# Kernel optimization log

Hardware: AMD Instinct MI355X
Metric: run time of the kernel (lower is better)

Reference implementation:

```python
import jax, jax.numpy as jnp
import numpy as np

SCALE = 0.125  # 1/sqrt(d_head)
QLEN, KLEN, BSZ, NHEAD, DHEAD = 1024, 1024, 4, 16, 64
RLEN = KLEN + 1


def rel_shift(x, klen):
    # x: [q, r, b, n] -> relative shift -> [q, klen, b, n]
    q, r, b, n = x.shape
    x = x.reshape(r, q, b, n)[1:]
    x = x.reshape(q, r - 1, b, n)[:, :klen]
    return x


def setup_inputs() -> dict:
    key = jax.random.key(0)
    ks = jax.random.split(key, 9)
    q_head = jax.random.normal(ks[0], (QLEN, BSZ, NHEAD, DHEAD), jnp.float32)
    k_head_h = jax.random.normal(ks[1], (KLEN, BSZ, NHEAD, DHEAD), jnp.float32)
    v_head_h = jax.random.normal(ks[2], (KLEN, BSZ, NHEAD, DHEAD), jnp.float32)
    k_head_r = jax.random.normal(ks[3], (RLEN, BSZ, NHEAD, DHEAD), jnp.float32)
    seg_embed = jax.random.normal(ks[4], (2, NHEAD, DHEAD), jnp.float32)
    seg_mat = jax.random.randint(ks[5], (QLEN, KLEN, BSZ), 0, 2) > 0  # bool
    r_w_bias = jax.random.normal(ks[6], (NHEAD, DHEAD), jnp.float32) * 0.02
    r_r_bias = jax.random.normal(ks[7], (NHEAD, DHEAD), jnp.float32) * 0.02
    r_s_bias = jax.random.normal(ks[8], (NHEAD, DHEAD), jnp.float32) * 0.02
    # causal mask: 1.0 where key position j is after query position i
    i = jnp.arange(QLEN)[:, None]
    j = jnp.arange(KLEN)[None, :]
    attn_mask = (j > i).astype(jnp.float32).reshape(QLEN, KLEN, 1, 1)
    return {
        "q_head": q_head, "k_head_h": k_head_h, "v_head_h": v_head_h,
        "k_head_r": k_head_r, "seg_embed": seg_embed, "seg_mat": seg_mat,
        "r_w_bias": r_w_bias, "r_r_bias": r_r_bias, "r_s_bias": r_s_bias,
        "attn_mask": attn_mask,
    }


def reference(q_head, k_head_h, v_head_h, k_head_r, seg_embed, seg_mat,
              r_w_bias, r_r_bias, r_s_bias, attn_mask):
    # content-based score: [q, k, b, n]
    ac = jnp.einsum('ibnd,jbnd->ijbn', q_head + r_w_bias, k_head_h)
    # position-based score, then relative shift
    bd = jnp.einsum('ibnd,jbnd->ijbn', q_head + r_r_bias, k_head_r)
    bd = rel_shift(bd, klen=ac.shape[1])
    # segment-based score: [q, 2, b, n] -> select same/diff per (i,j,b)
    ef = jnp.einsum('ibnd,snd->isbn', q_head + r_s_bias, seg_embed)
    ef = jnp.where(seg_mat[..., None], ef[:, 1:2], ef[:, 0:1])  # [q,k,b,n]
    attn_score = (ac + bd + ef) * SCALE
    attn_score = attn_score - 1e30 * attn_mask
    attn_prob = jax.nn.softmax(attn_score, axis=1)  # softmax over key axis j
    attn_vec = jnp.einsum('ijbn,jbnd->ibnd', attn_prob, v_head_h)
    return attn_vec
```

## Files before the change

### kernel.cpp

```cpp
#include <hip/hip_runtime.h>

#define QLEN  1024
#define KLEN  1024
#define BSZ   4
#define NHEAD 16
#define DHEAD 64
#define PS    4096
#define SCALE 0.125f
#define MSHIFT 16.0f

#define WK 72
#define WR 72
#define WV 68
#define WP 68

typedef __attribute__((ext_vector_type(8))) short  short8;
typedef __attribute__((ext_vector_type(4))) short  short4v;
typedef __attribute__((ext_vector_type(4))) float  float4v;

union S8 { short8 v; short4v h[2]; unsigned short u[8]; };

__device__ __forceinline__ unsigned short f2b(float f) {
    unsigned u; __builtin_memcpy(&u, &f, 4);
    return (unsigned short)((u + 0x8000u) >> 16);
}
__device__ __forceinline__ float b2f(unsigned short s) {
    unsigned u = ((unsigned)s) << 16;
    float f; __builtin_memcpy(&f, &u, 4);
    return f;
}

#define MFMA(a,b,c) __builtin_amdgcn_mfma_f32_16x16x32_bf16((a),(b),(c),0,0,0)

__global__ __launch_bounds__(256)
void seg_pack(const int4* __restrict__ sm4, unsigned long long* __restrict__ bits)
{
    int w  = (blockIdx.x << 2) + (threadIdx.x >> 6);
    int i  = w >> 4;
    int jw = w & 15;
    int jj = threadIdx.x & 63;
    int4 v = sm4[i*KLEN + (jw << 6) + jj];
    unsigned long long m0 = __ballot(v.x != 0);
    unsigned long long m1 = __ballot(v.y != 0);
    unsigned long long m2 = __ballot(v.z != 0);
    unsigned long long m3 = __ballot(v.w != 0);
    if (jj == 0) {
        unsigned long long* p = bits + (i << 6) + jw;
        p[0] = m0; p[16] = m1; p[32] = m2; p[48] = m3;
    }
}

__global__ __launch_bounds__(256, 3)
void relattn_mfma10(const float* __restrict__ q,
                    const float* __restrict__ kh,
                    const float* __restrict__ vh,
                    const float* __restrict__ kr,
                    const float* __restrict__ seg_embed,
                    const unsigned long long* __restrict__ segbits,
                    const float* __restrict__ rw,
                    const float* __restrict__ rr,
                    const float* __restrict__ rs,
                    float* __restrict__ out)
{
    __shared__ __align__(16) unsigned short sK [64*WK];
    __shared__ __align__(16) unsigned short sKr[128*WR];
    __shared__ __align__(16) unsigned short sVt[64*WV];
    __shared__ __align__(16) unsigned short sBD[64*WP];

    const int tid  = threadIdx.x;
    const int lane = tid & 63;
    const int wave = tid >> 6;
    const int quad = lane >> 4;
    const int l16  = lane & 15;
    const int bx   = blockIdx.x;
    const int h    = blockIdx.y;
    const int b    = h >> 4;
    const int n    = h & 15;
    const int qt   = (b & 1) ? bx : (15 - bx);
    const int i0   = qt << 6;
    const int m0   = wave << 4;
    const int hoff = h << 6;
    const int d0   = quad << 3;
    const int G0   = 961 - i0;
    const int srow = tid >> 4;
    const int c4   = (tid & 15) << 2;

    S8 aw0, aw1, ar0, ar1;
    float ef0r[4], ef1r[4];
    {
        float qv[16], rwv[16], rrv[16], rsv[16];
        const float* qp = q + (i0 + m0 + l16)*PS + hoff;
        *(float4*)&qv[0]  = *(const float4*)(qp + d0);
        *(float4*)&qv[4]  = *(const float4*)(qp + d0 + 4);
        *(float4*)&qv[8]  = *(const float4*)(qp + 32 + d0);
        *(float4*)&qv[12] = *(const float4*)(qp + 32 + d0 + 4);
        const float* rwp = rw + n*DHEAD;
        *(float4*)&rwv[0]  = *(const float4*)(rwp + d0);
        *(float4*)&rwv[4]  = *(const float4*)(rwp + d0 + 4);
        *(float4*)&rwv[8]  = *(const float4*)(rwp + 32 + d0);
        *(float4*)&rwv[12] = *(const float4*)(rwp + 32 + d0 + 4);
        const float* rrp = rr + n*DHEAD;
        *(float4*)&rrv[0]  = *(const float4*)(rrp + d0);
        *(float4*)&rrv[4]  = *(const float4*)(rrp + d0 + 4);
        *(float4*)&rrv[8]  = *(const float4*)(rrp + 32 + d0);
        *(float4*)&rrv[12] = *(const float4*)(rrp + 32 + d0 + 4);
        const float* rsp = rs + n*DHEAD;
        *(float4*)&rsv[0]  = *(const float4*)(rsp + d0);
        *(float4*)&rsv[4]  = *(const float4*)(rsp + d0 + 4);
        *(float4*)&rsv[8]  = *(const float4*)(rsp + 32 + d0);
        *(float4*)&rsv[12] = *(const float4*)(rsp + 32 + d0 + 4);

        #pragma unroll
        for (int mm = 0; mm < 8; ++mm) {
            aw0.u[mm] = f2b(qv[mm]   + rwv[mm]);
            aw1.u[mm] = f2b(qv[8+mm] + rwv[8+mm]);
            ar0.u[mm] = f2b(qv[mm]   + rrv[mm]);
            ar1.u[mm] = f2b(qv[8+mm] + rrv[8+mm]);
        }
        const float* se0 = seg_embed + n*DHEAD;
        const float* se1 = seg_embed + (NHEAD + n)*DHEAD;
        float e0 = 0.f, e1 = 0.f;
        #pragma unroll
        for (int mm = 0; mm < 8; ++mm) {
            float qs = qv[mm] + rsv[mm];
            e0 += qs * se0[d0 + mm];  e1 += qs * se1[d0 + mm];
            float qs2 = qv[8+mm] + rsv[8+mm];
            e0 += qs2 * se0[32 + d0 + mm];  e1 += qs2 * se1[32 + d0 + mm];
        }
        e0 += __shfl_xor(e0, 16); e0 += __shfl_xor(e0, 32);
        e1 += __shfl_xor(e1, 16); e1 += __shfl_xor(e1, 32);
        #pragma unroll
        for (int r = 0; r < 4; ++r) {
            ef0r[r] = __shfl(e0, (quad << 2) + r);
            ef1r[r] = __shfl(e1, (quad << 2) + r);
        }
    }

    {
        float4 t0[4], t1[4];
        #pragma unroll
        for (int k2 = 0; k2 < 4; ++k2) {
            int row = srow + (k2 << 4);
            t0[k2] = *(const float4*)(kh + row*PS + hoff + c4);
            t1[k2] = *(const float4*)(vh + row*PS + hoff + c4);
        }
        #pragma unroll
        for (int k2 = 0; k2 < 4; ++k2) {
            int row = srow + (k2 << 4);
            float4 kv = t0[k2];
            short4v kb = {(short)f2b(kv.x),(short)f2b(kv.y),(short)f2b(kv.z),(short)f2b(kv.w)};
            *(short4v*)&sK[row*WK + c4] = kb;
            float4 vv = t1[k2];
            sVt[(c4+0)*WV + row] = f2b(vv.x);
            sVt[(c4+1)*WV + row] = f2b(vv.y);
            sVt[(c4+2)*WV + row] = f2b(vv.z);
            sVt[(c4+3)*WV + row] = f2b(vv.w);
        }
    }
    {
        const float4 zf4 = make_float4(0.f, 0.f, 0.f, 0.f);
        float4 t0[4], t1[4];
        #pragma unroll
        for (int k2 = 0; k2 < 4; ++k2) {
            int row = srow + (k2 << 4);
            int g1 = G0 + row;
            t0[k2] = (g1 <= 1024) ? *(const float4*)(kr + g1*PS + hoff + c4) : zf4;
            int g2 = G0 + 64 + row;
            t1[k2] = (g2 <= 1024) ? *(const float4*)(kr + g2*PS + hoff + c4) : zf4;
        }
        #pragma unroll
        for (int k2 = 0; k2 < 4; ++k2) {
            int row = srow + (k2 << 4);
            float4 r1 = t0[k2];
            short4v rb1 = {(short)f2b(r1.x),(short)f2b(r1.y),(short)f2b(r1.z),(short)f2b(r1.w)};
            *(short4v*)&sKr[row*WR + c4] = rb1;
            float4 r2 = t1[k2];
            short4v rb2 = {(short)f2b(r2.x),(short)f2b(r2.y),(short)f2b(r2.z),(short)f2b(r2.w)};
            *(short4v*)&sKr[(64 + row)*WR + c4] = rb2;
        }
    }
    __syncthreads();

    float lp[4];
    float4v Ov[4];
    #pragma unroll
    for (int r = 0; r < 4; ++r) lp[r] = 0.f;
    #pragma unroll
    for (int cb = 0; cb < 4; ++cb) Ov[cb] = (float4v){0.f,0.f,0.f,0.f};

    for (int jt = 0; jt <= qt; ++jt) {
        const int  j0   = jt << 6;
        const bool diag = (jt == qt);
        const bool more = (jt < qt);
        const int  rot  = (jt & 1) << 2;

        float4 pK[4], pV[4], pR[4];
        if (more) {
            const int j0n = j0 + 64;
            const float4 zf4l = make_float4(0.f, 0.f, 0.f, 0.f);
            #pragma unroll
            for (int k2 = 0; k2 < 4; ++k2) {
                int row = srow + (k2 << 4);
                pK[k2] = *(const float4*)(kh + (j0n + row)*PS + hoff + c4);
                pV[k2] = *(const float4*)(vh + (j0n + row)*PS + hoff + c4);
                int g = G0 + ((jt + 2) << 6) + row;
                pR[k2] = (g <= 1024) ? *(const float4*)(kr + g*PS + hoff + c4) : zf4l;
            }
        }
        unsigned long long wbits[4];
        #pragma unroll
        for (int r = 0; r < 4; ++r) {
            int il = m0 + (quad << 2) + r;
            wbits[r] = segbits[(((i0+il) << 2) + b)*16 + jt] >> l16;
        }

        const int bbHi = diag ? wave : 3;
        float4v ac[4];
        #pragma unroll
        for (int bb = 0; bb < 4; ++bb) {
            ac[bb] = (float4v){0.f,0.f,0.f,0.f};
            if (bb <= bbHi) {
                const unsigned short* kp = &sK[((bb<<4) + l16)*WK + d0];
                short8 b0 = *(const short8*)kp;
                short8 b1 = *(const short8*)(kp + 32);
                ac[bb] = MFMA(aw0.v, b0, ac[bb]);
                ac[bb] = MFMA(aw1.v, b1, ac[bb]);
            }
        }

        const int cbLo = 3 - wave;
        const int cbHi = diag ? 3 : (7 - wave);
        #pragma unroll
        for (int cb = 0; cb < 8; ++cb) {
            if (cb >= cbLo && cb <= cbHi) {
                const unsigned short* rp = &sKr[((((cb + rot) & 7) << 4) + l16)*WR + d0];
                short8 b0 = *(const short8*)rp;
                short8 b1 = *(const short8*)(rp + 32);
                float4v z = (float4v){0.f,0.f,0.f,0.f};
                z = MFMA(ar0.v, b0, z);
                z = MFMA(ar1.v, b1, z);
                #pragma unroll
                for (int r = 0; r < 4; ++r) {
                    int il = m0 + (quad << 2) + r;
                    int jl = (cb << 4) + l16 - 63 + il;
                    if (jl >= 0 && jl < 64)
                        sBD[il*WP + jl] = f2b(z[r]);
                }
            }
        }

        #pragma unroll
        for (int r = 0; r < 4; ++r) {
            const int il = m0 + (quad << 2) + r;
            float psum = 0.f;
            #pragma unroll
            for (int bb = 0; bb < 4; ++bb) {
                const int jl = (bb << 4) + l16;
                float bd = b2f(sBD[il*WP + jl]);
                float ef = ((wbits[r] >> (bb << 4)) & 1ull) ? ef1r[r] : ef0r[r];
                float s  = (ac[bb][r] + bd + ef) * SCALE - MSHIFT;
                if (j0 + jl > i0 + il) s = -1e30f;
                float p = __expf(s);
                psum += p;
                sBD[il*WP + jl] = f2b(p);
            }
            lp[r] += psum;
        }

        {
            const unsigned short* pr = &sBD[(m0 + l16)*WP + d0];
            S8 pa0, pa1;
            pa0.h[0] = *(const short4v*)pr;
            pa0.h[1] = *(const short4v*)(pr + 4);
            pa1.h[0] = *(const short4v*)(pr + 32);
            pa1.h[1] = *(const short4v*)(pr + 36);
            const bool k2on = !(diag && wave < 2);
            #pragma unroll
            for (int cb = 0; cb < 4; ++cb) {
                const unsigned short* vp = &sVt[((cb<<4) + l16)*WV + d0];
                S8 v0, v1;
                v0.h[0] = *(const short4v*)vp;
                v0.h[1] = *(const short4v*)(vp + 4);
                Ov[cb] = MFMA(pa0.v, v0.v, Ov[cb]);
                if (k2on) {
                    v1.h[0] = *(const short4v*)(vp + 32);
                    v1.h[1] = *(const short4v*)(vp + 36);
                    Ov[cb] = MFMA(pa1.v, v1.v, Ov[cb]);
                }
            }
        }

        if (more) {
            __syncthreads();
            const int krslot = (jt & 1) << 6;
            #pragma unroll
            for (int k2 = 0; k2 < 4; ++k2) {
                int row = srow + (k2 << 4);
                float4 kv = pK[k2];
                short4v kb = {(short)f2b(kv.x),(short)f2b(kv.y),(short)f2b(kv.z),(short)f2b(kv.w)};
                *(short4v*)&sK[row*WK + c4] = kb;
                float4 vv = pV[k2];
                sVt[(c4+0)*WV + row] = f2b(vv.x);
                sVt[(c4+1)*WV + row] = f2b(vv.y);
                sVt[(c4+2)*WV + row] = f2b(vv.z);
                sVt[(c4+3)*WV + row] = f2b(vv.w);
                float4 rv = pR[k2];
                short4v rb = {(short)f2b(rv.x),(short)f2b(rv.y),(short)f2b(rv.z),(short)f2b(rv.w)};
                *(short4v*)&sKr[(krslot + row)*WR + c4] = rb;
            }
            __syncthreads();
        }
    }

    #pragma unroll
    for (int r = 0; r < 4; ++r) {
        float l = lp[r];
        l += __shfl_xor(l, 1);
        l += __shfl_xor(l, 2);
        l += __shfl_xor(l, 4);
        l += __shfl_xor(l, 8);
        const float inv = 1.f / l;
        const int il = m0 + (quad << 2) + r;
        #pragma unroll
        for (int cb = 0; cb < 4; ++cb)
            out[(i0+il)*PS + hoff + (cb<<4) + l16] = Ov[cb][r] * inv;
    }
}

extern "C" void kernel_launch(void* const* d_in, const int* in_sizes, int n_in,
                              void* d_out, int out_size, void* d_ws, size_t ws_size,
                              hipStream_t stream)
{
    const float* q  = (const float*)d_in[0];
    const float* kh = (const float*)d_in[1];
    const float* vh = (const float*)d_in[2];
    const float* kr = (const float*)d_in[3];
    const float* se = (const float*)d_in[4];
    const int*   sm = (const int*)  d_in[5];
    const float* rw = (const float*)d_in[6];
    const float* rr = (const float*)d_in[7];
    const float* rs = (const float*)d_in[8];
    float* o = (float*)d_out;
    unsigned long long* bits = (unsigned long long*)d_ws;
    (void)in_sizes; (void)n_in; (void)out_size; (void)ws_size;

    seg_pack<<<dim3(QLEN*16/4), 256, 0, stream>>>((const int4*)sm, bits);

    dim3 grid(QLEN/64, BSZ*NHEAD);
    relattn_mfma10<<<grid, 256, 0, stream>>>(q, kh, vh, kr, se, bits, rw, rr, rs, o);
}
```

Before: 290.1 us.

## Split long causal query tiles across two blocks with atomic combine and separate normalization

The attention kernel now uses a 1D grid of 1792 blocks. A lookup table assigns each block a query tile and, for tiles with qt>=4, one half of the key range. Split blocks accumulate unnormalized outputs and row sums with atomicAdd into buffers that seg_pack pre-zeroes, and a new norm_div kernel divides by the sums afterwards. The aim is better load balance under the causal triangle and shorter critical-path blocks. The cost is extra atomic traffic, a third kernel pass over the output, and redundant setup work in split blocks. It relies on the fixed MSHIFT softmax offset, so no max-rescaling between halves is needed.

```diff
diff --git a/kernel.cpp b/kernel.cpp
--- a/kernel.cpp
+++ b/kernel.cpp
@@ -32,8 +32,12 @@
 
 #define MFMA(a,b,c) __builtin_amdgcn_mfma_f32_16x16x32_bf16((a),(b),(c),0,0,0)
 
+__device__ const signed char QT_TAB[28] = {15,15,14,12, 13,13,14,10, 9,11,11,12, 7,9,8,2, 6,7,8,10, 5,6,1,3, 5,0,4,4};
+__device__ const signed char CH_TAB[28] = { 0, 1, 1, 1,  0, 1, 0, 1, 0, 0, 1, 0, 0,1,1,0, 1,1,0, 0, 0,0,0,0, 1,0,0,1};
+
 __global__ __launch_bounds__(256)
-void seg_pack(const int4* __restrict__ sm4, unsigned long long* __restrict__ bits)
+void seg_pack(const int4* __restrict__ sm4, unsigned long long* __restrict__ bits,
+              float4* __restrict__ out4, float4* __restrict__ lp4)
 {
     int w  = (blockIdx.x << 2) + (threadIdx.x >> 6);
     int i  = w >> 4;
@@ -48,10 +52,26 @@
         unsigned long long* p = bits + (i << 6) + jw;
         p[0] = m0; p[16] = m1; p[32] = m2; p[48] = m3;
     }
+    const float4 z4 = make_float4(0.f, 0.f, 0.f, 0.f);
+    out4[(blockIdx.x << 8) + threadIdx.x] = z4;
+    if (blockIdx.x < 64) lp4[(blockIdx.x << 8) + threadIdx.x] = z4;
+}
+
+__global__ __launch_bounds__(256)
+void norm_div(float4* __restrict__ out4, const float* __restrict__ lp)
+{
+    int idx = (blockIdx.x << 8) + threadIdx.x;
+    int i   = idx >> 10;
+    int col = (idx & 1023) << 2;
+    float l = lp[(i << 6) + (col >> 6)];
+    float4 v = out4[idx];
+    float inv = 1.f / l;
+    v.x *= inv; v.y *= inv; v.z *= inv; v.w *= inv;
+    out4[idx] = v;
 }
 
 __global__ __launch_bounds__(256, 3)
-void relattn_mfma10(const float* __restrict__ q,
+void relattn_mfma13(const float* __restrict__ q,
                     const float* __restrict__ kh,
                     const float* __restrict__ vh,
                     const float* __restrict__ kr,
@@ -60,7 +80,8 @@
                     const float* __restrict__ rw,
                     const float* __restrict__ rr,
                     const float* __restrict__ rs,
-                    float* __restrict__ out)
+                    float* __restrict__ out,
+                    float* __restrict__ lpart)
 {
     __shared__ __align__(16) unsigned short sK [64*WK];
     __shared__ __align__(16) unsigned short sKr[128*WR];
@@ -72,11 +93,20 @@
     const int wave = tid >> 6;
     const int quad = lane >> 4;
     const int l16  = lane & 15;
-    const int bx   = blockIdx.x;
-    const int h    = blockIdx.y;
-    const int b    = h >> 4;
-    const int n    = h & 15;
-    const int qt   = (b & 1) ? bx : (15 - bx);
+
+    const int id = blockIdx.x;
+    const int h  = id & 63;
+    const int s  = id >> 6;
+    const int b  = h >> 4;
+    const int n  = h & 15;
+
+    const int  qt   = QT_TAB[s];
+    const int  ch   = CH_TAB[s];
+    const bool dual = (qt >= 4);
+    const int  sp   = (qt + 1) >> 1;
+    const int  jt0  = (dual && ch)  ? sp       : 0;
+    const int  jtN  = (dual && !ch) ? (sp - 1) : qt;
+
     const int i0   = qt << 6;
     const int m0   = wave << 4;
     const int hoff = h << 6;
@@ -137,12 +167,13 @@
     }
 
     {
+        const int j0s = jt0 << 6;
         float4 t0[4], t1[4];
         #pragma unroll
         for (int k2 = 0; k2 < 4; ++k2) {
             int row = srow + (k2 << 4);
-            t0[k2] = *(const float4*)(kh + row*PS + hoff + c4);
-            t1[k2] = *(const float4*)(vh + row*PS + hoff + c4);
+            t0[k2] = *(const float4*)(kh + (j0s + row)*PS + hoff + c4);
+            t1[k2] = *(const float4*)(vh + (j0s + row)*PS + hoff + c4);
         }
         #pragma unroll
         for (int k2 = 0; k2 < 4; ++k2) {
@@ -159,13 +190,15 @@
     }
     {
         const float4 zf4 = make_float4(0.f, 0.f, 0.f, 0.f);
+        const int slotLo = (jt0 & 1) << 6;
+        const int slotHi = 64 - slotLo;
         float4 t0[4], t1[4];
         #pragma unroll
         for (int k2 = 0; k2 < 4; ++k2) {
             int row = srow + (k2 << 4);
-            int g1 = G0 + row;
+            int g1 = G0 + (jt0 << 6) + row;
             t0[k2] = (g1 <= 1024) ? *(const float4*)(kr + g1*PS + hoff + c4) : zf4;
-            int g2 = G0 + 64 + row;
+            int g2 = g1 + 64;
             t1[k2] = (g2 <= 1024) ? *(const float4*)(kr + g2*PS + hoff + c4) : zf4;
         }
         #pragma unroll
@@ -173,25 +206,25 @@
             int row = srow + (k2 << 4);
             float4 r1 = t0[k2];
             short4v rb1 = {(short)f2b(r1.x),(short)f2b(r1.y),(short)f2b(r1.z),(short)f2b(r1.w)};
-            *(short4v*)&sKr[row*WR + c4] = rb1;
+            *(short4v*)&sKr[(slotLo + row)*WR + c4] = rb1;
             float4 r2 = t1[k2];
             short4v rb2 = {(short)f2b(r2.x),(short)f2b(r2.y),(short)f2b(r2.z),(short)f2b(r2.w)};
-            *(short4v*)&sKr[(64 + row)*WR + c4] = rb2;
+            *(short4v*)&sKr[(slotHi + row)*WR + c4] = rb2;
         }
     }
     __syncthreads();
 
-    float lp[4];
+    float lsum[4];
     float4v Ov[4];
     #pragma unroll
-    for (int r = 0; r < 4; ++r) lp[r] = 0.f;
+    for (int r = 0; r < 4; ++r) lsum[r] = 0.f;
     #pragma unroll
     for (int cb = 0; cb < 4; ++cb) Ov[cb] = (float4v){0.f,0.f,0.f,0.f};
 
-    for (int jt = 0; jt <= qt; ++jt) {
+    for (int jt = jt0; jt <= jtN; ++jt) {
         const int  j0   = jt << 6;
         const bool diag = (jt == qt);
-        const bool more = (jt < qt);
+        const bool more = (jt < jtN);
         const int  rot  = (jt & 1) << 2;
 
         float4 pK[4], pV[4], pR[4];
@@ -258,13 +291,13 @@
                 const int jl = (bb << 4) + l16;
                 float bd = b2f(sBD[il*WP + jl]);
                 float ef = ((wbits[r] >> (bb << 4)) & 1ull) ? ef1r[r] : ef0r[r];
-                float s  = (ac[bb][r] + bd + ef) * SCALE - MSHIFT;
-                if (j0 + jl > i0 + il) s = -1e30f;
-                float p = __expf(s);
+                float s2 = (ac[bb][r] + bd + ef) * SCALE - MSHIFT;
+                if (j0 + jl > i0 + il) s2 = -1e30f;
+                float p = __expf(s2);
                 psum += p;
                 sBD[il*WP + jl] = f2b(p);
             }
-            lp[r] += psum;
+            lsum[r] += psum;
         }
 
         {
@@ -314,16 +347,21 @@
 
     #pragma unroll
     for (int r = 0; r < 4; ++r) {
-        float l = lp[r];
+        float l = lsum[r];
         l += __shfl_xor(l, 1);
         l += __shfl_xor(l, 2);
         l += __shfl_xor(l, 4);
         l += __shfl_xor(l, 8);
-        const float inv = 1.f / l;
         const int il = m0 + (quad << 2) + r;
-        #pragma unroll
-        for (int cb = 0; cb < 4; ++cb)
-            out[(i0+il)*PS + hoff + (cb<<4) + l16] = Ov[cb][r] * inv;
+        if (l16 == 0) {
+            float* lpp = lpart + (((i0 + il) << 6) + h);
+            if (dual) atomicAdd(lpp, l); else *lpp = l;
+        }
+        #pragma unroll
+        for (int cb = 0; cb < 4; ++cb) {
+            float* op = out + (i0+il)*PS + hoff + (cb<<4) + l16;
+            if (dual) atomicAdd(op, Ov[cb][r]); else *op = Ov[cb][r];
+        }
     }
 }
 
@@ -342,10 +380,14 @@
     const float* rs = (const float*)d_in[8];
     float* o = (float*)d_out;
     unsigned long long* bits = (unsigned long long*)d_ws;
+    float* lpart = (float*)((char*)d_ws + 524288);
     (void)in_sizes; (void)n_in; (void)out_size; (void)ws_size;
 
-    seg_pack<<<dim3(QLEN*16/4), 256, 0, stream>>>((const int4*)sm, bits);
-
-    dim3 grid(QLEN/64, BSZ*NHEAD);
-    relattn_mfma10<<<grid, 256, 0, stream>>>(q, kh, vh, kr, se, bits, rw, rr, rs, o);
-}
+    seg_pack<<<dim3(4096), 256, 0, stream>>>((const int4*)sm, bits,
+                                             (float4*)o, (float4*)lpart);
+
+    relattn_mfma13<<<dim3(1792), 256, 0, stream>>>(q, kh, vh, kr, se, bits,
+                                                   rw, rr, rs, o, lpart);
+
+    norm_div<<<dim3(4096), 256, 0, stream>>>((float4*)o, lpart);
+}
```

Result: slower. 320.6 us (+10.5%).

## Double-buffer K/V tiles and triple-buffer Kr to drop a per-tile barrier

Applied to the files above, without the earlier changes.

Splits the K and V shared tiles into ping-pong buffers and extends the relative-key buffer to three 64-row slots with rotating indices. The next tile can then be written without first waiting for all waves to finish reading the current one, removing one __syncthreads per iteration. The cost is more LDS per block and a launch bound lowered from 3 to 2 blocks, which reduces occupancy.

```diff
diff --git a/kernel.cpp b/kernel.cpp
--- a/kernel.cpp
+++ b/kernel.cpp
@@ -50,8 +50,8 @@
     }
 }
 
-__global__ __launch_bounds__(256, 3)
-void relattn_mfma10(const float* __restrict__ q,
+__global__ __launch_bounds__(256, 2)
+void relattn_mfma14(const float* __restrict__ q,
                     const float* __restrict__ kh,
                     const float* __restrict__ vh,
                     const float* __restrict__ kr,
@@ -62,9 +62,11 @@
                     const float* __restrict__ rs,
                     float* __restrict__ out)
 {
-    __shared__ __align__(16) unsigned short sK [64*WK];
-    __shared__ __align__(16) unsigned short sKr[128*WR];
-    __shared__ __align__(16) unsigned short sVt[64*WV];
+    __shared__ __align__(16) unsigned short sK0[64*WK];
+    __shared__ __align__(16) unsigned short sK1[64*WK];
+    __shared__ __align__(16) unsigned short sKr[192*WR];
+    __shared__ __align__(16) unsigned short sV0[64*WV];
+    __shared__ __align__(16) unsigned short sV1[64*WV];
     __shared__ __align__(16) unsigned short sBD[64*WP];
 
     const int tid  = threadIdx.x;
@@ -149,12 +151,12 @@
             int row = srow + (k2 << 4);
             float4 kv = t0[k2];
             short4v kb = {(short)f2b(kv.x),(short)f2b(kv.y),(short)f2b(kv.z),(short)f2b(kv.w)};
-            *(short4v*)&sK[row*WK + c4] = kb;
+            *(short4v*)&sK0[row*WK + c4] = kb;
             float4 vv = t1[k2];
-            sVt[(c4+0)*WV + row] = f2b(vv.x);
-            sVt[(c4+1)*WV + row] = f2b(vv.y);
-            sVt[(c4+2)*WV + row] = f2b(vv.z);
-            sVt[(c4+3)*WV + row] = f2b(vv.w);
+            sV0[(c4+0)*WV + row] = f2b(vv.x);
+            sV0[(c4+1)*WV + row] = f2b(vv.y);
+            sV0[(c4+2)*WV + row] = f2b(vv.z);
+            sV0[(c4+3)*WV + row] = f2b(vv.w);
         }
     }
     {
@@ -188,11 +190,19 @@
     #pragma unroll
     for (int cb = 0; cb < 4; ++cb) Ov[cb] = (float4v){0.f,0.f,0.f,0.f};
 
+    bool cur = false;
+    int  s0  = 0;
+
     for (int jt = 0; jt <= qt; ++jt) {
         const int  j0   = jt << 6;
         const bool diag = (jt == qt);
         const bool more = (jt < qt);
-        const int  rot  = (jt & 1) << 2;
+        unsigned short* sKc = cur ? sK1 : sK0;
+        unsigned short* sVc = cur ? sV1 : sV0;
+        unsigned short* sKn = cur ? sK0 : sK1;
+        unsigned short* sVn = cur ? sV0 : sV1;
+        const int sHi = (s0 == 2) ? 0 : s0 + 1;
+        const int s2  = (s0 == 0) ? 2 : s0 - 1;
 
         float4 pK[4], pV[4], pR[4];
         if (more) {
@@ -220,7 +230,7 @@
         for (int bb = 0; bb < 4; ++bb) {
             ac[bb] = (float4v){0.f,0.f,0.f,0.f};
             if (bb <= bbHi) {
-                const unsigned short* kp = &sK[((bb<<4) + l16)*WK + d0];
+                const unsigned short* kp = &sKc[((bb<<4) + l16)*WK + d0];
                 short8 b0 = *(const short8*)kp;
                 short8 b1 = *(const short8*)(kp + 32);
                 ac[bb] = MFMA(aw0.v, b0, ac[bb]);
@@ -233,7 +243,9 @@
         #pragma unroll
         for (int cb = 0; cb < 8; ++cb) {
             if (cb >= cbLo && cb <= cbHi) {
-                const unsigned short* rp = &sKr[((((cb + rot) & 7) << 4) + l16)*WR + d0];
+                const int slot = (cb < 4) ? s0 : sHi;
+                const int rrow = (slot << 6) + ((cb & 3) << 4) + l16;
+                const unsigned short* rp = &sKr[rrow*WR + d0];
                 short8 b0 = *(const short8*)rp;
                 short8 b1 = *(const short8*)(rp + 32);
                 float4v z = (float4v){0.f,0.f,0.f,0.f};
@@ -277,7 +289,7 @@
             const bool k2on = !(diag && wave < 2);
             #pragma unroll
             for (int cb = 0; cb < 4; ++cb) {
-                const unsigned short* vp = &sVt[((cb<<4) + l16)*WV + d0];
+                const unsigned short* vp = &sVc[((cb<<4) + l16)*WV + d0];
                 S8 v0, v1;
                 v0.h[0] = *(const short4v*)vp;
                 v0.h[1] = *(const short4v*)(vp + 4);
@@ -291,25 +303,25 @@
         }
 
         if (more) {
-            __syncthreads();
-            const int krslot = (jt & 1) << 6;
             #pragma unroll
             for (int k2 = 0; k2 < 4; ++k2) {
                 int row = srow + (k2 << 4);
                 float4 kv = pK[k2];
                 short4v kb = {(short)f2b(kv.x),(short)f2b(kv.y),(short)f2b(kv.z),(short)f2b(kv.w)};
-                *(short4v*)&sK[row*WK + c4] = kb;
+                *(short4v*)&sKn[row*WK + c4] = kb;
                 float4 vv = pV[k2];
-                sVt[(c4+0)*WV + row] = f2b(vv.x);
-                sVt[(c4+1)*WV + row] = f2b(vv.y);
-                sVt[(c4+2)*WV + row] = f2b(vv.z);
-                sVt[(c4+3)*WV + row] = f2b(vv.w);
+                sVn[(c4+0)*WV + row] = f2b(vv.x);
+                sVn[(c4+1)*WV + row] = f2b(vv.y);
+                sVn[(c4+2)*WV + row] = f2b(vv.z);
+                sVn[(c4+3)*WV + row] = f2b(vv.w);
                 float4 rv = pR[k2];
                 short4v rb = {(short)f2b(rv.x),(short)f2b(rv.y),(short)f2b(rv.z),(short)f2b(rv.w)};
-                *(short4v*)&sKr[(krslot + row)*WR + c4] = rb;
+                *(short4v*)&sKr[(( s2 << 6) + row)*WR + c4] = rb;
             }
             __syncthreads();
         }
+        cur = !cur;
+        s0  = (s0 == 2) ? 0 : s0 + 1;
     }
 
     #pragma unroll
@@ -347,5 +359,5 @@
     seg_pack<<<dim3(QLEN*16/4), 256, 0, stream>>>((const int4*)sm, bits);
 
     dim3 grid(QLEN/64, BSZ*NHEAD);
-    relattn_mfma10<<<grid, 256, 0, stream>>>(q, kh, vh, kr, se, bits, rw, rr, rs, o);
-}
+    relattn_mfma14<<<grid, 256, 0, stream>>>(q, kh, vh, kr, se, bits, rw, rr, rs, o);
+}
```

New measurement: 240.5 us. 17.1% less time.
